# Performance work log

Hardware: AMD Instinct MI355X
Metric: run time of the kernel (lower is better)

The kernel has to match this reference:

```python
import jax, jax.numpy as jnp
import numpy as np

NUM_EMBEDDINGS = 1024
EMBEDDING_DIM = 64
SCALE = 1.0 / NUM_EMBEDDINGS


def setup_inputs() -> dict:
    key = jax.random.key(0)
    k1, k2 = jax.random.split(key)
    input = jax.random.normal(k1, (16, EMBEDDING_DIM, 64, 64), dtype=jnp.float32)
    # nn.Embedding weight initialized uniform(-scale, scale)
    codebook = jax.random.uniform(k2, (NUM_EMBEDDINGS, EMBEDDING_DIM),
                                  dtype=jnp.float32, minval=-SCALE, maxval=SCALE)
    return {"input": input, "codebook": codebook}


def reference(input, codebook):
    # NCHW -> NHWC, flatten spatial+batch to tokens [N, D]
    x = jnp.transpose(input, (0, 2, 3, 1))           # [B, H, W, D]
    B, H, W, D = x.shape
    flat = x.reshape(-1, D)                          # [N, D]
    dists = (jnp.sum(flat ** 2, axis=1, keepdims=True)
             + jnp.sum(codebook ** 2, axis=1)
             - 2.0 * flat @ codebook.T)              # [N, K]
    idx = jnp.argmin(dists, axis=-1).reshape(B, H, W)  # [B, H, W]
    quantized = codebook[idx]                        # [B, H, W, D]
    return jnp.transpose(quantized, (0, 3, 1, 2))    # [B, D, H, W]
```

## Files before the change

### kernel.cpp

```cpp
#include <hip/hip_runtime.h>

typedef short short8 __attribute__((ext_vector_type(8)));
typedef float f32x4 __attribute__((ext_vector_type(4)));
typedef unsigned long long u64;

#define NE 1024
#define D 64
#define HW 4096
#define MARGIN 3.0e-3f
#define FLT_MAX_F 3.402823466e+38f
#define MSTRIDE 17

#define WS_BN  0
#define WS_EBF 4096

__device__ __forceinline__ unsigned short f2bf(float f) {
    unsigned u = __float_as_uint(f);
    return (unsigned short)((u + 0x7fffu + ((u >> 16) & 1u)) >> 16);
}

__device__ __forceinline__ float np_sum64_sq(const float* v) {
    float s[8];
#pragma unroll
    for (int j = 0; j < 8; ++j) s[j] = __fmul_rn(v[j], v[j]);
#pragma unroll
    for (int i = 8; i < 64; i += 8) {
#pragma unroll
        for (int j = 0; j < 8; ++j)
            s[j] = __fadd_rn(s[j], __fmul_rn(v[i + j], v[i + j]));
    }
    return __fadd_rn(__fadd_rn(__fadd_rn(s[0], s[1]), __fadd_rn(s[2], s[3])),
                     __fadd_rn(__fadd_rn(s[4], s[5]), __fadd_rn(s[6], s[7])));
}

__global__ __launch_bounds__(256) void kP_prep(
        const float* __restrict__ cb, float* __restrict__ bn,
        unsigned short* __restrict__ ebf) {
    const int gid = blockIdx.x * 256 + threadIdx.x;
    ebf[gid] = f2bf(cb[gid]);
    if (gid < NE) {
        float row[D];
        const float4* r4 = reinterpret_cast<const float4*>(cb + (size_t)gid * D);
#pragma unroll
        for (int i = 0; i < 16; ++i) {
            float4 v = r4[i];
            row[4*i+0] = v.x; row[4*i+1] = v.y; row[4*i+2] = v.z; row[4*i+3] = v.w;
        }
        bn[gid] = np_sum64_sq(row);
    }
}

__global__ __launch_bounds__(256, 4) void k_mega(
        const float* __restrict__ in, const unsigned short* __restrict__ ebf,
        const float* __restrict__ bn_g, const float* __restrict__ cb,
        float* __restrict__ out) {
    __shared__ unsigned short ebq[128 * 64];
    __shared__ float sbn[NE];
    __shared__ u64 lmask[128 * MSTRIDE];
    __shared__ unsigned short win_s[128];

    const int tid  = threadIdx.x;
    const int lane = tid & 63, w = tid >> 6;
    const int lcol = lane & 15, lhi = lane >> 4, lrow = lhi * 4;
    const int tokw = blockIdx.x * 128 + w * 32;
    const int b = tokw >> 12, hwb = tokw & 4095;

#pragma unroll
    for (int i = 0; i < 4; ++i) sbn[tid + i * 256] = bn_g[tid + i * 256];

    const float* xbase = in + (size_t)b * (D * HW);
    const int hw0 = hwb + lcol, hw1 = hw0 + 16;
    const int kb = lhi * 8;
    short8 B00, B01, B10, B11;
    {
        const float* p;
        p = xbase + (size_t)kb * HW + hw0;
#pragma unroll
        for (int j = 0; j < 8; ++j) B00[j] = (short)f2bf(p[(size_t)j * HW]);
        p = xbase + (size_t)(kb + 32) * HW + hw0;
#pragma unroll
        for (int j = 0; j < 8; ++j) B01[j] = (short)f2bf(p[(size_t)j * HW]);
        p = xbase + (size_t)kb * HW + hw1;
#pragma unroll
        for (int j = 0; j < 8; ++j) B10[j] = (short)f2bf(p[(size_t)j * HW]);
        p = xbase + (size_t)(kb + 32) * HW + hw1;
#pragma unroll
        for (int j = 0; j < 8; ++j) B11[j] = (short)f2bf(p[(size_t)j * HW]);
    }

    const int swz   = (lcol & 7) << 4;
    const int aoff0 = lcol * 128 + ((lhi * 16) ^ swz);
    const int aoff1 = lcol * 128 + ((64 + lhi * 16) ^ swz);

    int4 pf0, pf1, pf2, pf3;
#define LOADC(C) { const int4* s_ = (const int4*)(ebf + (size_t)(C) * 8192);  \
                   pf0 = s_[tid]; pf1 = s_[tid + 256];                        \
                   pf2 = s_[tid + 512]; pf3 = s_[tid + 768]; }
#define WRITEC() { int4 t_[4] = {pf0, pf1, pf2, pf3};                         \
    _Pragma("unroll")                                                         \
    for (int i = 0; i < 4; ++i) {                                             \
        int L = (tid + i * 256) * 16;                                         \
        int row = L >> 7, wi = L & 127;                                       \
        *(int4*)((char*)ebq + row * 128 + (wi ^ ((row & 7) << 4))) = t_[i];   \
    } }

#define CHUNK_MFMA(C, CT)                                                     \
    const char* lp = (const char*)ebq + (CT) * 2048;                          \
    short8 A0 = *(const short8*)(lp + aoff0);                                 \
    short8 A1 = *(const short8*)(lp + aoff1);                                 \
    f32x4 bnv = *(const f32x4*)(sbn + (C) * 128 + (CT) * 16 + lrow);          \
    f32x4 acc = {0.f, 0.f, 0.f, 0.f};                                         \
    acc = __builtin_amdgcn_mfma_f32_16x16x32_bf16(A0, B00, acc, 0, 0, 0);     \
    acc = __builtin_amdgcn_mfma_f32_16x16x32_bf16(A1, B01, acc, 0, 0, 0);     \
    f32x4 ac2 = {0.f, 0.f, 0.f, 0.f};                                         \
    ac2 = __builtin_amdgcn_mfma_f32_16x16x32_bf16(A0, B10, ac2, 0, 0, 0);     \
    ac2 = __builtin_amdgcn_mfma_f32_16x16x32_bf16(A1, B11, ac2, 0, 0, 0);

    float v10 = FLT_MAX_F, v11 = FLT_MAX_F;
    LOADC(0)
    for (int c = 0; c < 8; ++c) {
        __syncthreads();
        WRITEC()
        __syncthreads();
        LOADC(c < 7 ? c + 1 : 0)
#pragma unroll
        for (int ct = 0; ct < 8; ++ct) {
            CHUNK_MFMA(c, ct)
#pragma unroll
            for (int r = 0; r < 4; ++r) {
                v10 = fminf(v10, __fmaf_rn(-2.0f, acc[r], bnv[r]));
                v11 = fminf(v11, __fmaf_rn(-2.0f, ac2[r], bnv[r]));
            }
        }
    }
    v10 = fminf(v10, __shfl_xor(v10, 16)); v10 = fminf(v10, __shfl_xor(v10, 32));
    v11 = fminf(v11, __shfl_xor(v11, 16)); v11 = fminf(v11, __shfl_xor(v11, 32));
    const float thr0 = v10 + MARGIN, thr1 = v11 + MARGIN;
    const int tA = w * 32 + lcol, tB = tA + 16;

    for (int c = 0; c < 8; ++c) {
        __syncthreads();
        WRITEC()
        __syncthreads();
        if (c < 7) LOADC(c + 1)
        u64 w0a = 0, w1a = 0, w0b = 0, w1b = 0;
#pragma unroll
        for (int ct = 0; ct < 8; ++ct) {
            CHUNK_MFMA(c, ct)
#pragma unroll
            for (int r = 0; r < 4; ++r) {
                const int bit = (ct & 3) * 16 + lrow + r;
                float t0 = __fmaf_rn(-2.0f, acc[r], bnv[r]);
                if (t0 <= thr0) { if (ct < 4) w0a |= 1ull << bit; else w1a |= 1ull << bit; }
                float t1 = __fmaf_rn(-2.0f, ac2[r], bnv[r]);
                if (t1 <= thr1) { if (ct < 4) w0b |= 1ull << bit; else w1b |= 1ull << bit; }
            }
        }
        w0a |= __shfl_xor(w0a, 16); w0a |= __shfl_xor(w0a, 32);
        w1a |= __shfl_xor(w1a, 16); w1a |= __shfl_xor(w1a, 32);
        w0b |= __shfl_xor(w0b, 16); w0b |= __shfl_xor(w0b, 32);
        w1b |= __shfl_xor(w1b, 16); w1b |= __shfl_xor(w1b, 32);
        if (lhi == 0) {
            lmask[tA * MSTRIDE + 2 * c]     = w0a;
            lmask[tA * MSTRIDE + 2 * c + 1] = w1a;
            lmask[tB * MSTRIDE + 2 * c]     = w0b;
            lmask[tB * MSTRIDE + 2 * c + 1] = w1b;
        }
    }
    __syncthreads();

    {
        const int tok_l = tid >> 1, sub = tid & 1;
        const int tok = blockIdx.x * 128 + tok_l;
        const int tb = tok >> 12, thw = tok & 4095;
        const float* x = in + (size_t)tb * (D * HW) + thw;
        float xv[D];
#pragma unroll
        for (int d = 0; d < D; ++d) xv[d] = x[(size_t)d * HW];
        const float a = np_sum64_sq(xv);

        u64 best = ~0ull;
        int kp = -1;
        int pos = 0;
        for (int wd = 0; wd < 16; ++wd) {
            u64 m = lmask[tok_l * MSTRIDE + wd];
            while (m) {
                const int k = wd * 64 + (int)__builtin_ctzll(m);
                m &= m - 1;
                if (((pos++) & 1) != sub) continue;
                if (kp < 0) { kp = k; continue; }
                const float* e0 = cb + (size_t)kp * D;
                const float* e1 = cb + (size_t)k * D;
                float d0 = 0.f, d1 = 0.f;
#pragma unroll
                for (int d = 0; d < 64; ++d) {
                    d0 = __fmaf_rn(xv[d], e0[d], d0);
                    d1 = __fmaf_rn(xv[d], e1[d], d1);
                }
                float q0 = __fsub_rn(__fadd_rn(a, bn_g[kp]), __fmul_rn(2.0f, d0));
                float q1 = __fsub_rn(__fadd_rn(a, bn_g[k]),  __fmul_rn(2.0f, d1));
                u64 key0 = (((u64)__float_as_uint(q0)) << 32) | (unsigned)kp;
                u64 key1 = (((u64)__float_as_uint(q1)) << 32) | (unsigned)k;
                u64 kmin = key0 < key1 ? key0 : key1;
                best = best < kmin ? best : kmin;
                kp = -1;
            }
        }
        if (kp >= 0) {
            const float* e0 = cb + (size_t)kp * D;
            float d0 = 0.f;
#pragma unroll
            for (int d = 0; d < 64; ++d) d0 = __fmaf_rn(xv[d], e0[d], d0);
            float q0 = __fsub_rn(__fadd_rn(a, bn_g[kp]), __fmul_rn(2.0f, d0));
            u64 key0 = (((u64)__float_as_uint(q0)) << 32) | (unsigned)kp;
            best = best < key0 ? best : key0;
        }
        {
            u64 v = __shfl_xor(best, 1);
            best = best < v ? best : v;
        }
        if (sub == 0) win_s[tok_l] = (unsigned short)(best & 0x3FFull);
    }
    __syncthreads();

    {
        const int tok_l = tid >> 1, half = tid & 1;
        const int tok = blockIdx.x * 128 + tok_l;
        const int gb = tok >> 12, ghw = tok & 4095;
        const unsigned k = win_s[tok_l];
        const float4* er = reinterpret_cast<const float4*>(cb + (size_t)k * D + half * 32);
        float* ot = out + (size_t)gb * (D * HW) + ghw;
#pragma unroll
        for (int i = 0; i < 8; ++i) {
            float4 e = er[i];
            ot[(size_t)(half * 32 + 4*i + 0) * HW] = e.x;
            ot[(size_t)(half * 32 + 4*i + 1) * HW] = e.y;
            ot[(size_t)(half * 32 + 4*i + 2) * HW] = e.z;
            ot[(size_t)(half * 32 + 4*i + 3) * HW] = e.w;
        }
    }
}

extern "C" void kernel_launch(void* const* d_in, const int* in_sizes, int n_in,
                              void* d_out, int out_size, void* d_ws, size_t ws_size,
                              hipStream_t stream) {
    const float* in  = (const float*)d_in[0];
    const float* cb  = (const float*)d_in[1];
    float*       out = (float*)d_out;
    char*        ws  = (char*)d_ws;

    float*          bn  = (float*)(ws + WS_BN);
    unsigned short* ebf = (unsigned short*)(ws + WS_EBF);

    hipLaunchKernelGGL(kP_prep, dim3(256), dim3(256), 0, stream, cb, bn, ebf);
    hipLaunchKernelGGL(k_mega,  dim3(512), dim3(256), 0, stream, in, ebf, bn, cb, out);
}
```

Measured before the change: 76.21 us.

## Double-buffer codebook LDS chunks and fold norm bias into MFMA accumulator

Doubles the shared-memory codebook buffer so the next chunk is written into the alternate buffer after compute, removing one of the two barriers per chunk. The codebook norm is pre-scaled by -0.5 and used as the MFMA accumulator's initial value, so the per-element FMA before each min becomes a plain max, and the threshold test becomes a direct compare. Occupancy hint drops from 4 to 2 blocks per CU to accommodate the larger LDS footprint, and the rescaled comparison may change candidate selection slightly at the margin.

```diff
diff --git a/kernel.cpp b/kernel.cpp
--- a/kernel.cpp
+++ b/kernel.cpp
@@ -50,11 +50,11 @@
     }
 }
 
-__global__ __launch_bounds__(256, 4) void k_mega(
+__global__ __launch_bounds__(256, 2) void k_mega(
         const float* __restrict__ in, const unsigned short* __restrict__ ebf,
         const float* __restrict__ bn_g, const float* __restrict__ cb,
         float* __restrict__ out) {
-    __shared__ unsigned short ebq[128 * 64];
+    __shared__ unsigned short ebq[2 * 128 * 64];
     __shared__ float sbn[NE];
     __shared__ u64 lmask[128 * MSTRIDE];
     __shared__ unsigned short win_s[128];
@@ -66,7 +66,8 @@
     const int b = tokw >> 12, hwb = tokw & 4095;
 
 #pragma unroll
-    for (int i = 0; i < 4; ++i) sbn[tid + i * 256] = bn_g[tid + i * 256];
+    for (int i = 0; i < 4; ++i)
+        sbn[tid + i * 256] = __fmul_rn(-0.5f, bn_g[tid + i * 256]);
 
     const float* xbase = in + (size_t)b * (D * HW);
     const int hw0 = hwb + lcol, hw1 = hw0 + 16;
@@ -96,64 +97,70 @@
 #define LOADC(C) { const int4* s_ = (const int4*)(ebf + (size_t)(C) * 8192);  \
                    pf0 = s_[tid]; pf1 = s_[tid + 256];                        \
                    pf2 = s_[tid + 512]; pf3 = s_[tid + 768]; }
-#define WRITEC() { int4 t_[4] = {pf0, pf1, pf2, pf3};                         \
+#define WRITEC(BUF) { int4 t_[4] = {pf0, pf1, pf2, pf3};                      \
     _Pragma("unroll")                                                         \
     for (int i = 0; i < 4; ++i) {                                             \
         int L = (tid + i * 256) * 16;                                         \
         int row = L >> 7, wi = L & 127;                                       \
-        *(int4*)((char*)ebq + row * 128 + (wi ^ ((row & 7) << 4))) = t_[i];   \
+        *(int4*)((char*)ebq + (BUF) * 16384 + row * 128                       \
+                 + (wi ^ ((row & 7) << 4))) = t_[i];                          \
     } }
 
-#define CHUNK_MFMA(C, CT)                                                     \
-    const char* lp = (const char*)ebq + (CT) * 2048;                          \
+#define CHUNK_MFMA(BUF, C, CT)                                                \
+    const char* lp = (const char*)ebq + (BUF) * 16384 + (CT) * 2048;          \
     short8 A0 = *(const short8*)(lp + aoff0);                                 \
     short8 A1 = *(const short8*)(lp + aoff1);                                 \
-    f32x4 bnv = *(const f32x4*)(sbn + (C) * 128 + (CT) * 16 + lrow);          \
-    f32x4 acc = {0.f, 0.f, 0.f, 0.f};                                         \
+    f32x4 cin = *(const f32x4*)(sbn + (C) * 128 + (CT) * 16 + lrow);          \
+    f32x4 acc = cin;                                                          \
     acc = __builtin_amdgcn_mfma_f32_16x16x32_bf16(A0, B00, acc, 0, 0, 0);     \
     acc = __builtin_amdgcn_mfma_f32_16x16x32_bf16(A1, B01, acc, 0, 0, 0);     \
-    f32x4 ac2 = {0.f, 0.f, 0.f, 0.f};                                         \
+    f32x4 ac2 = cin;                                                          \
     ac2 = __builtin_amdgcn_mfma_f32_16x16x32_bf16(A0, B10, ac2, 0, 0, 0);     \
     ac2 = __builtin_amdgcn_mfma_f32_16x16x32_bf16(A1, B11, ac2, 0, 0, 0);
 
-    float v10 = FLT_MAX_F, v11 = FLT_MAX_F;
+    f32x4 vA = {-FLT_MAX_F, -FLT_MAX_F, -FLT_MAX_F, -FLT_MAX_F};
+    f32x4 vB = vA;
     LOADC(0)
+    WRITEC(0)
+    __syncthreads();
     for (int c = 0; c < 8; ++c) {
+        const int buf = c & 1;
+        if (c < 7) LOADC(c + 1)
+#pragma unroll
+        for (int ct = 0; ct < 8; ++ct) {
+            CHUNK_MFMA(buf, c, ct)
+#pragma unroll
+            for (int r = 0; r < 4; ++r) {
+                vA[r] = fmaxf(vA[r], acc[r]);
+                vB[r] = fmaxf(vB[r], ac2[r]);
+            }
+        }
+        if (c < 7) WRITEC(buf ^ 1)
         __syncthreads();
-        WRITEC()
-        __syncthreads();
-        LOADC(c < 7 ? c + 1 : 0)
-#pragma unroll
-        for (int ct = 0; ct < 8; ++ct) {
-            CHUNK_MFMA(c, ct)
-#pragma unroll
-            for (int r = 0; r < 4; ++r) {
-                v10 = fminf(v10, __fmaf_rn(-2.0f, acc[r], bnv[r]));
-                v11 = fminf(v11, __fmaf_rn(-2.0f, ac2[r], bnv[r]));
-            }
-        }
-    }
-    v10 = fminf(v10, __shfl_xor(v10, 16)); v10 = fminf(v10, __shfl_xor(v10, 32));
-    v11 = fminf(v11, __shfl_xor(v11, 16)); v11 = fminf(v11, __shfl_xor(v11, 32));
-    const float thr0 = v10 + MARGIN, thr1 = v11 + MARGIN;
+    }
+    float v0 = fmaxf(fmaxf(vA[0], vA[1]), fmaxf(vA[2], vA[3]));
+    float v1 = fmaxf(fmaxf(vB[0], vB[1]), fmaxf(vB[2], vB[3]));
+    v0 = fmaxf(v0, __shfl_xor(v0, 16)); v0 = fmaxf(v0, __shfl_xor(v0, 32));
+    v1 = fmaxf(v1, __shfl_xor(v1, 16)); v1 = fmaxf(v1, __shfl_xor(v1, 32));
+    const float athr0 = v0 - 0.5f * MARGIN;
+    const float athr1 = v1 - 0.5f * MARGIN;
     const int tA = w * 32 + lcol, tB = tA + 16;
 
+    LOADC(0)
+    WRITEC(0)
+    __syncthreads();
     for (int c = 0; c < 8; ++c) {
-        __syncthreads();
-        WRITEC()
-        __syncthreads();
+        const int buf = c & 1;
         if (c < 7) LOADC(c + 1)
         u64 w0a = 0, w1a = 0, w0b = 0, w1b = 0;
 #pragma unroll
         for (int ct = 0; ct < 8; ++ct) {
-            CHUNK_MFMA(c, ct)
+            CHUNK_MFMA(buf, c, ct)
 #pragma unroll
             for (int r = 0; r < 4; ++r) {
                 const int bit = (ct & 3) * 16 + lrow + r;
-                float t0 = __fmaf_rn(-2.0f, acc[r], bnv[r]);
-                if (t0 <= thr0) { if (ct < 4) w0a |= 1ull << bit; else w1a |= 1ull << bit; }
-                float t1 = __fmaf_rn(-2.0f, ac2[r], bnv[r]);
-                if (t1 <= thr1) { if (ct < 4) w0b |= 1ull << bit; else w1b |= 1ull << bit; }
+                if (acc[r] >= athr0) { if (ct < 4) w0a |= 1ull << bit; else w1a |= 1ull << bit; }
+                if (ac2[r] >= athr1) { if (ct < 4) w0b |= 1ull << bit; else w1b |= 1ull << bit; }
             }
         }
         w0a |= __shfl_xor(w0a, 16); w0a |= __shfl_xor(w0a, 32);
@@ -166,8 +173,9 @@
             lmask[tB * MSTRIDE + 2 * c]     = w0b;
             lmask[tB * MSTRIDE + 2 * c + 1] = w1b;
         }
-    }
-    __syncthreads();
+        if (c < 7) WRITEC(buf ^ 1)
+        __syncthreads();
+    }
 
     {
         const int tok_l = tid >> 1, sub = tid & 1;
```

Result: no change. 75.24 us (-1.3%).

## Fuse the two-pass codebook scan into one pass with running-max candidate masks

Applied to the files above, without the earlier changes.

Folds -0.5*||e||^2 into the MFMA accumulator init, so each token now takes the max of x·e - 0.5||e||^2 instead of the min of a distance. Each chunk's scores stay in registers and are masked against a running threshold built from the chunks seen so far. This drops the second MFMA pass and the second reload of the bf16 codebook into LDS. Blocks now cover 64 tokens (grid doubled), and the exact fp32 re-rank and the output write are split over 4 threads per token. The risk is that thresholds taken from early chunks are looser, so more candidates may reach the exact re-rank.

```diff
diff --git a/kernel.cpp b/kernel.cpp
--- a/kernel.cpp
+++ b/kernel.cpp
@@ -56,22 +56,23 @@
         float* __restrict__ out) {
     __shared__ unsigned short ebq[128 * 64];
     __shared__ float sbn[NE];
-    __shared__ u64 lmask[128 * MSTRIDE];
-    __shared__ unsigned short win_s[128];
+    __shared__ u64 lmask[64 * MSTRIDE];
+    __shared__ unsigned short win_s[64];
 
     const int tid  = threadIdx.x;
     const int lane = tid & 63, w = tid >> 6;
     const int lcol = lane & 15, lhi = lane >> 4, lrow = lhi * 4;
-    const int tokw = blockIdx.x * 128 + w * 32;
+    const int tokw = blockIdx.x * 64 + w * 16;
     const int b = tokw >> 12, hwb = tokw & 4095;
 
 #pragma unroll
-    for (int i = 0; i < 4; ++i) sbn[tid + i * 256] = bn_g[tid + i * 256];
+    for (int i = 0; i < 4; ++i)
+        sbn[tid + i * 256] = __fmul_rn(-0.5f, bn_g[tid + i * 256]);
 
     const float* xbase = in + (size_t)b * (D * HW);
-    const int hw0 = hwb + lcol, hw1 = hw0 + 16;
+    const int hw0 = hwb + lcol;
     const int kb = lhi * 8;
-    short8 B00, B01, B10, B11;
+    short8 B00, B01;
     {
         const float* p;
         p = xbase + (size_t)kb * HW + hw0;
@@ -80,12 +81,6 @@
         p = xbase + (size_t)(kb + 32) * HW + hw0;
 #pragma unroll
         for (int j = 0; j < 8; ++j) B01[j] = (short)f2bf(p[(size_t)j * HW]);
-        p = xbase + (size_t)kb * HW + hw1;
-#pragma unroll
-        for (int j = 0; j < 8; ++j) B10[j] = (short)f2bf(p[(size_t)j * HW]);
-        p = xbase + (size_t)(kb + 32) * HW + hw1;
-#pragma unroll
-        for (int j = 0; j < 8; ++j) B11[j] = (short)f2bf(p[(size_t)j * HW]);
     }
 
     const int swz   = (lcol & 7) << 4;
@@ -104,74 +99,61 @@
         *(int4*)((char*)ebq + row * 128 + (wi ^ ((row & 7) << 4))) = t_[i];   \
     } }
 
-#define CHUNK_MFMA(C, CT)                                                     \
-    const char* lp = (const char*)ebq + (CT) * 2048;                          \
-    short8 A0 = *(const short8*)(lp + aoff0);                                 \
-    short8 A1 = *(const short8*)(lp + aoff1);                                 \
-    f32x4 bnv = *(const f32x4*)(sbn + (C) * 128 + (CT) * 16 + lrow);          \
-    f32x4 acc = {0.f, 0.f, 0.f, 0.f};                                         \
-    acc = __builtin_amdgcn_mfma_f32_16x16x32_bf16(A0, B00, acc, 0, 0, 0);     \
-    acc = __builtin_amdgcn_mfma_f32_16x16x32_bf16(A1, B01, acc, 0, 0, 0);     \
-    f32x4 ac2 = {0.f, 0.f, 0.f, 0.f};                                         \
-    ac2 = __builtin_amdgcn_mfma_f32_16x16x32_bf16(A0, B10, ac2, 0, 0, 0);     \
-    ac2 = __builtin_amdgcn_mfma_f32_16x16x32_bf16(A1, B11, ac2, 0, 0, 0);
-
-    float v10 = FLT_MAX_F, v11 = FLT_MAX_F;
+    f32x4 vA = {-FLT_MAX_F, -FLT_MAX_F, -FLT_MAX_F, -FLT_MAX_F};
+    const int tl = w * 16 + lcol;
+    float acc32[32];
+
     LOADC(0)
+    WRITEC()
+    __syncthreads();
     for (int c = 0; c < 8; ++c) {
-        __syncthreads();
-        WRITEC()
-        __syncthreads();
-        LOADC(c < 7 ? c + 1 : 0)
+        if (c < 7) LOADC(c + 1)
 #pragma unroll
         for (int ct = 0; ct < 8; ++ct) {
-            CHUNK_MFMA(c, ct)
+            const char* lp = (const char*)ebq + ct * 2048;
+            short8 A0 = *(const short8*)(lp + aoff0);
+            short8 A1 = *(const short8*)(lp + aoff1);
+            f32x4 acc = *(const f32x4*)(sbn + c * 128 + ct * 16 + lrow);
+            acc = __builtin_amdgcn_mfma_f32_16x16x32_bf16(A0, B00, acc, 0, 0, 0);
+            acc = __builtin_amdgcn_mfma_f32_16x16x32_bf16(A1, B01, acc, 0, 0, 0);
 #pragma unroll
             for (int r = 0; r < 4; ++r) {
-                v10 = fminf(v10, __fmaf_rn(-2.0f, acc[r], bnv[r]));
-                v11 = fminf(v11, __fmaf_rn(-2.0f, ac2[r], bnv[r]));
+                acc32[ct * 4 + r] = acc[r];
+                vA[r] = fmaxf(vA[r], acc[r]);
             }
         }
-    }
-    v10 = fminf(v10, __shfl_xor(v10, 16)); v10 = fminf(v10, __shfl_xor(v10, 32));
-    v11 = fminf(v11, __shfl_xor(v11, 16)); v11 = fminf(v11, __shfl_xor(v11, 32));
-    const float thr0 = v10 + MARGIN, thr1 = v11 + MARGIN;
-    const int tA = w * 32 + lcol, tB = tA + 16;
-
-    for (int c = 0; c < 8; ++c) {
-        __syncthreads();
-        WRITEC()
-        __syncthreads();
-        if (c < 7) LOADC(c + 1)
-        u64 w0a = 0, w1a = 0, w0b = 0, w1b = 0;
+        float v0 = fmaxf(fmaxf(vA[0], vA[1]), fmaxf(vA[2], vA[3]));
+        v0 = fmaxf(v0, __shfl_xor(v0, 16));
+        v0 = fmaxf(v0, __shfl_xor(v0, 32));
+        const float athr = v0 - 0.5f * MARGIN;
+        u64 w0 = 0, w1 = 0;
 #pragma unroll
         for (int ct = 0; ct < 8; ++ct) {
-            CHUNK_MFMA(c, ct)
 #pragma unroll
             for (int r = 0; r < 4; ++r) {
                 const int bit = (ct & 3) * 16 + lrow + r;
-                float t0 = __fmaf_rn(-2.0f, acc[r], bnv[r]);
-                if (t0 <= thr0) { if (ct < 4) w0a |= 1ull << bit; else w1a |= 1ull << bit; }
-                float t1 = __fmaf_rn(-2.0f, ac2[r], bnv[r]);
-                if (t1 <= thr1) { if (ct < 4) w0b |= 1ull << bit; else w1b |= 1ull << bit; }
+                if (acc32[ct * 4 + r] >= athr) {
+                    if (ct < 4) w0 |= 1ull << bit; else w1 |= 1ull << bit;
+                }
             }
         }
-        w0a |= __shfl_xor(w0a, 16); w0a |= __shfl_xor(w0a, 32);
-        w1a |= __shfl_xor(w1a, 16); w1a |= __shfl_xor(w1a, 32);
-        w0b |= __shfl_xor(w0b, 16); w0b |= __shfl_xor(w0b, 32);
-        w1b |= __shfl_xor(w1b, 16); w1b |= __shfl_xor(w1b, 32);
+        w0 |= __shfl_xor(w0, 16); w0 |= __shfl_xor(w0, 32);
+        w1 |= __shfl_xor(w1, 16); w1 |= __shfl_xor(w1, 32);
         if (lhi == 0) {
-            lmask[tA * MSTRIDE + 2 * c]     = w0a;
-            lmask[tA * MSTRIDE + 2 * c + 1] = w1a;
-            lmask[tB * MSTRIDE + 2 * c]     = w0b;
-            lmask[tB * MSTRIDE + 2 * c + 1] = w1b;
+            lmask[tl * MSTRIDE + 2 * c]     = w0;
+            lmask[tl * MSTRIDE + 2 * c + 1] = w1;
+        }
+        __syncthreads();
+        if (c < 7) {
+            WRITEC()
+            __syncthreads();
         }
     }
     __syncthreads();
 
     {
-        const int tok_l = tid >> 1, sub = tid & 1;
-        const int tok = blockIdx.x * 128 + tok_l;
+        const int tok_l = tid >> 2, sub = tid & 3;
+        const int tok = blockIdx.x * 64 + tok_l;
         const int tb = tok >> 12, thw = tok & 4095;
         const float* x = in + (size_t)tb * (D * HW) + thw;
         float xv[D];
@@ -187,7 +169,7 @@
             while (m) {
                 const int k = wd * 64 + (int)__builtin_ctzll(m);
                 m &= m - 1;
-                if (((pos++) & 1) != sub) continue;
+                if (((pos++) & 3) != sub) continue;
                 if (kp < 0) { kp = k; continue; }
                 const float* e0 = cb + (size_t)kp * D;
                 const float* e1 = cb + (size_t)k * D;
@@ -215,8 +197,9 @@
             u64 key0 = (((u64)__float_as_uint(q0)) << 32) | (unsigned)kp;
             best = best < key0 ? best : key0;
         }
-        {
-            u64 v = __shfl_xor(best, 1);
+#pragma unroll
+        for (int o = 1; o < 4; o <<= 1) {
+            u64 v = __shfl_xor(best, o);
             best = best < v ? best : v;
         }
         if (sub == 0) win_s[tok_l] = (unsigned short)(best & 0x3FFull);
@@ -224,19 +207,19 @@
     __syncthreads();
 
     {
-        const int tok_l = tid >> 1, half = tid & 1;
-        const int tok = blockIdx.x * 128 + tok_l;
+        const int tok_l = tid >> 2, qd = (tid & 3) << 4;
+        const int tok = blockIdx.x * 64 + tok_l;
         const int gb = tok >> 12, ghw = tok & 4095;
         const unsigned k = win_s[tok_l];
-        const float4* er = reinterpret_cast<const float4*>(cb + (size_t)k * D + half * 32);
+        const float4* er = reinterpret_cast<const float4*>(cb + (size_t)k * D + qd);
         float* ot = out + (size_t)gb * (D * HW) + ghw;
 #pragma unroll
-        for (int i = 0; i < 8; ++i) {
+        for (int i = 0; i < 4; ++i) {
             float4 e = er[i];
-            ot[(size_t)(half * 32 + 4*i + 0) * HW] = e.x;
-            ot[(size_t)(half * 32 + 4*i + 1) * HW] = e.y;
-            ot[(size_t)(half * 32 + 4*i + 2) * HW] = e.z;
-            ot[(size_t)(half * 32 + 4*i + 3) * HW] = e.w;
+            ot[(size_t)(qd + 4*i + 0) * HW] = e.x;
+            ot[(size_t)(qd + 4*i + 1) * HW] = e.y;
+            ot[(size_t)(qd + 4*i + 2) * HW] = e.z;
+            ot[(size_t)(qd + 4*i + 3) * HW] = e.w;
         }
     }
 }
@@ -252,6 +235,6 @@
     float*          bn  = (float*)(ws + WS_BN);
     unsigned short* ebf = (unsigned short*)(ws + WS_EBF);
 
-    hipLaunchKernelGGL(kP_prep, dim3(256), dim3(256), 0, stream, cb, bn, ebf);
-    hipLaunchKernelGGL(k_mega,  dim3(512), dim3(256), 0, stream, in, ebf, bn, cb, out);
-}
+    hipLaunchKernelGGL(kP_prep, dim3(256),  dim3(256), 0, stream, cb, bn, ebf);
+    hipLaunchKernelGGL(k_mega,  dim3(1024), dim3(256), 0, stream, in, ebf, bn, cb, out);
+}
```

Result: slower. 128.8 us (+69.0%).
